# Kernel optimization log

Hardware: AMD Instinct MI355X
Metric: run time of the kernel (lower is better)

## Reference

```python
import jax, jax.numpy as jnp
import numpy as np

B, S, M = 32, 16384, 64
IN_DIM, OUT_DIM, HID = 64, 64, 512
N_READ, N_WRITE = 1, 1
LSTM_IN = IN_DIM + OUT_DIM + M * N_READ
EPS = 1e-8  # torch F.cosine_similarity eps


def setup_inputs():
    key = jax.random.key(0)
    ks = jax.random.split(key, 16)
    w = lambda k, sh: (0.02 * jax.random.normal(k, sh)).astype(jnp.float32)
    return {
        'x_input': jax.random.normal(ks[0], (B, 1, IN_DIM), dtype=jnp.float32),
        'prev_desired_output': jax.random.normal(ks[1], (B, 1, OUT_DIM), dtype=jnp.float32),
        'prev_read_vec': jax.random.normal(ks[2], (B, 1, M * N_READ), dtype=jnp.float32),
        'memory': jax.random.normal(ks[3], (B, S, M), dtype=jnp.float32),
        'W_ih': w(ks[4], (4 * HID, LSTM_IN)),
        'W_hh': w(ks[5], (4 * HID, HID)),
        'b_ih': jnp.zeros((4 * HID,), jnp.float32),
        'b_hh': jnp.zeros((4 * HID,), jnp.float32),
        'W_r': w(ks[6], (N_READ * (M + 6), HID)),
        'b_r': jnp.zeros((N_READ * (M + 6),), jnp.float32),
        'W_w': w(ks[7], (N_WRITE * (3 * M + 6), HID)),
        'b_w': jnp.zeros((N_WRITE * (3 * M + 6),), jnp.float32),
        'W_o': w(ks[8], (OUT_DIM, HID + M * N_READ)),
        'b_o': jnp.zeros((OUT_DIM,), jnp.float32),
    }


def _addressing(h, W, b, mem, nbr_heads, is_read):
    # ctrl2head linear -> [B, H, gate_dim], then slice k/beta/g/s/gamma(/erase/add)
    out = (h @ W.T + b).reshape(h.shape[0], nbr_heads, -1)
    k = out[..., :M]
    beta = jax.nn.softplus(out[..., M:M + 1])
    g = jax.nn.sigmoid(out[..., M + 1:M + 2])
    s = jax.nn.softmax(jax.nn.softplus(out[..., M + 2:M + 5]), axis=-1)  # 3-tap shift kernel
    gamma = 1.0 + jax.nn.softplus(out[..., M + 5:M + 6])
    # content addressing: cosine similarity of key vs each slot
    dot = jnp.einsum('bhm,bsm->bhs', k, mem)
    kn = jnp.maximum(jnp.linalg.norm(k, axis=-1), EPS)   # [B,H]
    mn = jnp.maximum(jnp.linalg.norm(mem, axis=-1), EPS)  # [B,S]
    cos = dot / (kn[:, :, None] * mn[:, None, :])
    wc = jax.nn.softmax(beta * cos, axis=-1)
    # location addressing; prev_w is zeros after reset so wg = g*wc + (1-g)*0
    wg = g * wc
    # circular 3-tap shift (conv1d over circularly padded weights)
    ws = s[..., 0:1] * jnp.roll(wg, 1, axis=-1) + s[..., 1:2] * wg + s[..., 2:3] * jnp.roll(wg, -1, axis=-1)
    wgam = ws ** gamma  # sharpening
    w_final = wgam / jnp.sum(wgam, axis=-1, keepdims=True)
    if is_read:
        return w_final
    return w_final, out[..., M + 6:2 * M + 6], out[..., 2 * M + 6:3 * M + 6]


def reference(x_input, prev_desired_output, prev_read_vec, memory,
              W_ih, W_hh, b_ih, b_hh, W_r, b_r, W_w, b_w, W_o, b_o):
    # single-layer LSTM step from zero (h0, c0) = (0, 0)
    xt = jnp.concatenate([x_input, prev_desired_output, prev_read_vec], axis=2)[:, 0]
    z = xt @ W_ih.T + b_ih + b_hh  # h0 @ W_hh.T == 0
    i, f, gg, o = jnp.split(z, 4, axis=-1)
    c = jax.nn.sigmoid(i) * jnp.tanh(gg)  # c0 == 0
    h = jax.nn.sigmoid(o) * jnp.tanh(c)   # [B, HID]
    # read heads (read pre-write memory)
    w_read = _addressing(h, W_r, b_r, memory, N_READ, True)
    r = jnp.einsum('bhs,bsm->bhm', w_read, memory)  # [B, N_READ, M]
    # write heads: source per-head loop overwrites nmemory[bidx] each head,
    # so only the LAST write head takes effect -> use head -1
    w_write, erase, add = _addressing(h, W_w, b_w, memory, N_WRITE, False)
    wl, el, al = w_write[:, -1], erase[:, -1], add[:, -1]
    new_mem = memory * (1.0 - wl[:, :, None] * el[:, None, :]) + wl[:, :, None] * al[:, None, :]
    # external output: softmax(Linear(cat(h, read)))
    ext_in = jnp.concatenate([h, r.reshape(r.shape[0], -1)], axis=-1)
    output = jax.nn.softmax(ext_in @ W_o.T + b_o, axis=-1)
    return output, new_mem
```

## Files before the change

kernel.cpp:

```cpp
#include <hip/hip_runtime.h>
#include <hip/hip_bf16.h>
#include <math.h>

#define BB 32
#define SS 16384
#define MM 64
#define HID 512
#define EPSV 1e-8f

#define OFF_H   0
#define OFF_P   16384
#define OFF_SER 32768
#define OFF_SEW 32800
#define OFF_SGR 32832
#define OFF_SGW 32864
#define OFF_R   32896
#define OFF_ER  40960
#define OFF_EW  (OFF_ER + BB*SS)
#define OFF_WGR (OFF_EW + BB*SS)
#define OFF_WGW (OFF_WGR + BB*SS)

__device__ __forceinline__ float sigmoidf_(float x) { return 1.f / (1.f + expf(-x)); }
__device__ __forceinline__ float softplusf_(float x) {
    return (x > 0.f) ? x + log1pf(expf(-x)) : log1pf(expf(x));
}

__global__ void k_lstm(const float* __restrict__ x, const float* __restrict__ pdo,
                       const float* __restrict__ prv,
                       const float* __restrict__ W_ih, const float* __restrict__ b_ih,
                       const float* __restrict__ b_hh, float* __restrict__ ws) {
    if (blockIdx.x == 0) {
        for (int i = threadIdx.x; i < 128 + BB * MM; i += 256) ws[OFF_SER + i] = 0.f;
    }
    int wid = blockIdx.x * 4 + (threadIdx.x >> 6);
    int lane = threadIdx.x & 63;
    int b = wid >> 9, t = wid & 511;
    float x0 = x[b * 64 + lane];
    float x1 = pdo[b * 64 + lane];
    float x2 = prv[b * 64 + lane];
    const float* wi = W_ih + (size_t)t * 192;
    const float* wg = W_ih + (size_t)(1024 + t) * 192;
    const float* wo = W_ih + (size_t)(1536 + t) * 192;
    float zi = x0 * wi[lane] + x1 * wi[64 + lane] + x2 * wi[128 + lane];
    float zg = x0 * wg[lane] + x1 * wg[64 + lane] + x2 * wg[128 + lane];
    float zo = x0 * wo[lane] + x1 * wo[64 + lane] + x2 * wo[128 + lane];
    #pragma unroll
    for (int off = 32; off >= 1; off >>= 1) {
        zi += __shfl_xor(zi, off);
        zg += __shfl_xor(zg, off);
        zo += __shfl_xor(zo, off);
    }
    if (lane == 0) {
        zi += b_ih[t] + b_hh[t];
        zg += b_ih[1024 + t] + b_hh[1024 + t];
        zo += b_ih[1536 + t] + b_hh[1536 + t];
        float c = sigmoidf_(zi) * tanhf(zg);
        ws[OFF_H + (size_t)b * 512 + t] = sigmoidf_(zo) * tanhf(c);
    }
}

__global__ void k_heads(const float* __restrict__ W_r, const float* __restrict__ b_r,
                        const float* __restrict__ W_w, const float* __restrict__ b_w,
                        float* __restrict__ ws) {
    int wid = blockIdx.x * 4 + (threadIdx.x >> 6);
    int lane = threadIdx.x & 63;
    int b = wid / 268, j = wid % 268;
    const float* h = ws + OFF_H + (size_t)b * 512;
    const float* wrow;
    float bias;
    if (j < 70) { wrow = W_r + (size_t)j * 512; bias = b_r[j]; }
    else        { wrow = W_w + (size_t)(j - 70) * 512; bias = b_w[j - 70]; }
    float acc = 0.f;
    #pragma unroll
    for (int c = 0; c < 8; c++) acc = fmaf(h[c * 64 + lane], wrow[c * 64 + lane], acc);
    #pragma unroll
    for (int off = 32; off >= 1; off >>= 1) acc += __shfl_xor(acc, off);
    if (lane != 0) return;
    acc += bias;
    float* P = ws + OFF_P + (size_t)b * 512;
    if (j < 70) {
        if (j < 64)       P[j] = acc;
        else if (j == 64) P[64] = softplusf_(acc);
        else if (j == 65) P[65] = sigmoidf_(acc);
        else if (j <= 68) P[96 + (j - 66)] = acc;
        else              P[69] = 1.f + softplusf_(acc);
    } else {
        int jj = j - 70;
        if (jj < 64)       P[128 + jj] = acc;
        else if (jj == 64) P[192] = softplusf_(acc);
        else if (jj == 65) P[193] = sigmoidf_(acc);
        else if (jj <= 68) P[224 + (jj - 66)] = acc;
        else if (jj == 69) P[197] = 1.f + softplusf_(acc);
        else if (jj < 134) P[256 + (jj - 70)] = acc;
        else               P[320 + (jj - 134)] = acc;
    }
}

__global__ void k_scorewgam(const float* __restrict__ mem, float* __restrict__ ws) {
    int b = blockIdx.x >> 6;
    int chunk = blockIdx.x & 63;
    int tid = threadIdx.x;
    const float* P = ws + OFF_P + (size_t)b * 512;

    __shared__ float sh_kr[64], sh_kw[64];
    __shared__ float sh_er[258], sh_ew[258];
    __shared__ float par[8];
    __shared__ float lr[4], lw[4];

    if (tid < 64) {
        float kr = P[tid], kw = P[128 + tid];
        sh_kr[tid] = kr; sh_kw[tid] = kw;
        float nr = kr * kr, nw = kw * kw;
        #pragma unroll
        for (int off = 32; off >= 1; off >>= 1) {
            nr += __shfl_xor(nr, off);
            nw += __shfl_xor(nw, off);
        }
        if (tid == 0) {
            par[0] = 1.f / fmaxf(sqrtf(nr), EPSV);
            par[1] = 1.f / fmaxf(sqrtf(nw), EPSV);
            float s0 = softplusf_(P[96]), s1 = softplusf_(P[97]), s2 = softplusf_(P[98]);
            float mx = fmaxf(s0, fmaxf(s1, s2));
            float e0 = expf(s0 - mx), e1 = expf(s1 - mx), e2 = expf(s2 - mx);
            float si = 1.f / (e0 + e1 + e2);
            par[2] = e0 * si; par[3] = e1 * si; par[4] = e2 * si;
            s0 = softplusf_(P[224]); s1 = softplusf_(P[225]); s2 = softplusf_(P[226]);
            mx = fmaxf(s0, fmaxf(s1, s2));
            e0 = expf(s0 - mx); e1 = expf(s1 - mx); e2 = expf(s2 - mx);
            si = 1.f / (e0 + e1 + e2);
            par[5] = e0 * si; par[6] = e1 * si; par[7] = e2 * si;
        }
    }
    float beta_r = P[64], beta_w = P[192];
    float gamma_r = P[69], gamma_w = P[197];
    __syncthreads();
    float ikr = par[0], ikw = par[1];

    int row0 = chunk * 256;
    {
        const float4* mrow = (const float4*)(mem + ((size_t)b * SS + row0 + tid) * 64);
        float dr = 0.f, dw = 0.f, n2 = 0.f;
        #pragma unroll
        for (int k = 0; k < 16; k++) {
            float4 m4 = mrow[k];
            float4 kr4 = *(const float4*)(sh_kr + k * 4);
            float4 kw4 = *(const float4*)(sh_kw + k * 4);
            dr = fmaf(m4.x, kr4.x, fmaf(m4.y, kr4.y, fmaf(m4.z, kr4.z, fmaf(m4.w, kr4.w, dr))));
            dw = fmaf(m4.x, kw4.x, fmaf(m4.y, kw4.y, fmaf(m4.z, kw4.z, fmaf(m4.w, kw4.w, dw))));
            n2 = fmaf(m4.x, m4.x, fmaf(m4.y, m4.y, fmaf(m4.z, m4.z, fmaf(m4.w, m4.w, n2))));
        }
        float imn = 1.f / fmaxf(sqrtf(n2), EPSV);
        sh_er[1 + tid] = exp2f(1.44269504f * beta_r * (dr * ikr * imn - 1.f));
        sh_ew[1 + tid] = exp2f(1.44269504f * beta_w * (dw * ikw * imn - 1.f));
    }
    if (tid < 32) {
        int grp = tid >> 4, c = tid & 15;
        int hrow = grp ? ((row0 + 256) & (SS - 1)) : ((row0 - 1) & (SS - 1));
        float4 m4 = *(const float4*)(mem + ((size_t)b * SS + hrow) * 64 + c * 4);
        float4 kr4 = *(const float4*)(sh_kr + c * 4);
        float4 kw4 = *(const float4*)(sh_kw + c * 4);
        float dr = m4.x * kr4.x + m4.y * kr4.y + m4.z * kr4.z + m4.w * kr4.w;
        float dw = m4.x * kw4.x + m4.y * kw4.y + m4.z * kw4.z + m4.w * kw4.w;
        float n2 = m4.x * m4.x + m4.y * m4.y + m4.z * m4.z + m4.w * m4.w;
        #pragma unroll
        for (int off = 8; off >= 1; off >>= 1) {
            dr += __shfl_xor(dr, off);
            dw += __shfl_xor(dw, off);
            n2 += __shfl_xor(n2, off);
        }
        if (c == 0) {
            float imn = 1.f / fmaxf(sqrtf(n2), EPSV);
            int slot = grp ? 257 : 0;
            sh_er[slot] = exp2f(1.44269504f * beta_r * (dr * ikr * imn - 1.f));
            sh_ew[slot] = exp2f(1.44269504f * beta_w * (dw * ikw * imn - 1.f));
        }
    }
    __syncthreads();

    float cvr = par[2] * sh_er[tid] + par[3] * sh_er[tid + 1] + par[4] * sh_er[tid + 2];
    float cvw = par[5] * sh_ew[tid] + par[6] * sh_ew[tid + 1] + par[7] * sh_ew[tid + 2];
    float wgr = exp2f(gamma_r * log2f(cvr));
    float wgw = exp2f(gamma_w * log2f(cvw));
    ws[OFF_WGR + (size_t)b * SS + row0 + tid] = wgr;
    ws[OFF_WGW + (size_t)b * SS + row0 + tid] = wgw;

    float rr = wgr, rw = wgw;
    #pragma unroll
    for (int off = 32; off >= 1; off >>= 1) {
        rr += __shfl_xor(rr, off);
        rw += __shfl_xor(rw, off);
    }
    int wv = tid >> 6, ln = tid & 63;
    if (ln == 0) { lr[wv] = rr; lw[wv] = rw; }
    __syncthreads();
    if (tid == 0) {
        atomicAdd(ws + OFF_SGR + b, lr[0] + lr[1] + lr[2] + lr[3]);
        atomicAdd(ws + OFF_SGW + b, lw[0] + lw[1] + lw[2] + lw[3]);
    }
}

__global__ void k_update(const float* __restrict__ mem, float* __restrict__ ws,
                         float* __restrict__ out) {
    int b = blockIdx.x >> 6, chunk = blockIdx.x & 63, tid = threadIdx.x;
    int rowslot = tid >> 4, col = tid & 15;
    const float* P = ws + OFF_P + (size_t)b * 512;
    float4 er4 = *(const float4*)(P + 256 + col * 4);
    float4 ad4 = *(const float4*)(P + 320 + col * 4);
    float isr = 1.f / ws[OFF_SGR + b];
    float isw = 1.f / ws[OFF_SGW + b];
    const float* wgr = ws + OFF_WGR + (size_t)b * SS;
    const float* wgw = ws + OFF_WGW + (size_t)b * SS;
    float* nm = out + 2048 + (size_t)b * SS * 64;
    float4 racc = {0.f, 0.f, 0.f, 0.f};
    int row0 = chunk * 256;
    for (int it = 0; it < 16; ++it) {
        int row = row0 + it * 16 + rowslot;
        float wr = wgr[row] * isr;
        float ww = wgw[row] * isw;
        float4 v = *(const float4*)(mem + ((size_t)b * SS + row) * 64 + col * 4);
        racc.x = fmaf(wr, v.x, racc.x);
        racc.y = fmaf(wr, v.y, racc.y);
        racc.z = fmaf(wr, v.z, racc.z);
        racc.w = fmaf(wr, v.w, racc.w);
        float4 o4;
        o4.x = v.x * (1.f - ww * er4.x) + ww * ad4.x;
        o4.y = v.y * (1.f - ww * er4.y) + ww * ad4.y;
        o4.z = v.z * (1.f - ww * er4.z) + ww * ad4.z;
        o4.w = v.w * (1.f - ww * er4.w) + ww * ad4.w;
        *(float4*)(nm + (size_t)row * 64 + col * 4) = o4;
    }
    __shared__ float4 red[256];
    red[tid] = racc;
    __syncthreads();
    if (tid < 16) {
        float4 a = red[tid];
        for (int rs = 1; rs < 16; ++rs) {
            float4 t2 = red[rs * 16 + tid];
            a.x += t2.x; a.y += t2.y; a.z += t2.z; a.w += t2.w;
        }
        atomicAdd(ws + OFF_R + b * 64 + tid * 4 + 0, a.x);
        atomicAdd(ws + OFF_R + b * 64 + tid * 4 + 1, a.y);
        atomicAdd(ws + OFF_R + b * 64 + tid * 4 + 2, a.z);
        atomicAdd(ws + OFF_R + b * 64 + tid * 4 + 3, a.w);
    }
}

__global__ void k_out(const float* __restrict__ ws, const float* __restrict__ W_o,
                      const float* __restrict__ b_o, float* __restrict__ out) {
    int b = blockIdx.x, o = threadIdx.x;
    const float* h = ws + OFF_H + (size_t)b * 512;
    const float* r = ws + OFF_R + (size_t)b * 64;
    const float* w = W_o + (size_t)o * 576;
    float acc = b_o[o];
    for (int t = 0; t < 512; t++) acc = fmaf(h[t], w[t], acc);
    for (int m = 0; m < 64; m++) acc = fmaf(r[m], w[512 + m], acc);
    float mx = acc;
    #pragma unroll
    for (int off = 32; off >= 1; off >>= 1) mx = fmaxf(mx, __shfl_xor(mx, off));
    float e = expf(acc - mx);
    float sm = e;
    #pragma unroll
    for (int off = 32; off >= 1; off >>= 1) sm += __shfl_xor(sm, off);
    out[b * 64 + o] = e / sm;
}

extern "C" void kernel_launch(void* const* d_in, const int* in_sizes, int n_in,
                              void* d_out, int out_size, void* d_ws, size_t ws_size,
                              hipStream_t stream) {
    const float* x    = (const float*)d_in[0];
    const float* pdo  = (const float*)d_in[1];
    const float* prv  = (const float*)d_in[2];
    const float* mem  = (const float*)d_in[3];
    const float* W_ih = (const float*)d_in[4];
    const float* b_ih = (const float*)d_in[6];
    const float* b_hh = (const float*)d_in[7];
    const float* W_r  = (const float*)d_in[8];
    const float* b_r  = (const float*)d_in[9];
    const float* W_w  = (const float*)d_in[10];
    const float* b_w  = (const float*)d_in[11];
    const float* W_o  = (const float*)d_in[12];
    const float* b_o  = (const float*)d_in[13];
    float* out = (float*)d_out;
    float* ws  = (float*)d_ws;

    k_lstm<<<BB * 512 / 4, 256, 0, stream>>>(x, pdo, prv, W_ih, b_ih, b_hh, ws);
    k_heads<<<(BB * 268) / 4, 256, 0, stream>>>(W_r, b_r, W_w, b_w, ws);
    k_scorewgam<<<BB * 64, 256, 0, stream>>>(mem, ws);
    k_update<<<BB * 64, 256, 0, stream>>>(mem, ws, out);
    k_out<<<BB, 64, 0, stream>>>(ws, W_o, b_o, out);
}
```

Baseline: 115.5 us.

## Coalesce scoring memory reads and replace atomics with per-chunk partial reductions

In the scoring kernel, each memory row is now read by 4 adjacent lanes, each loading 16 floats, with shuffle reductions. Before, one thread read a whole 256-byte row, so accesses across a wavefront were strided. The global atomicAdd accumulations for the weight sums and read vectors become per-chunk partial buffers that the consumer kernels sum. This also removes the zero-init step in the LSTM kernel. The cost is extra shuffles and a small serial reduction over 64 chunks in k_update and k_out.

```diff
diff --git a/kernel.cpp b/kernel.cpp
--- a/kernel.cpp
+++ b/kernel.cpp
@@ -8,17 +8,13 @@
 #define HID 512
 #define EPSV 1e-8f
 
-#define OFF_H   0
-#define OFF_P   16384
-#define OFF_SER 32768
-#define OFF_SEW 32800
-#define OFF_SGR 32832
-#define OFF_SGW 32864
-#define OFF_R   32896
-#define OFF_ER  40960
-#define OFF_EW  (OFF_ER + BB*SS)
-#define OFF_WGR (OFF_EW + BB*SS)
-#define OFF_WGW (OFF_WGR + BB*SS)
+#define OFF_H    0
+#define OFF_P    16384
+#define OFF_SGRP 32768
+#define OFF_SGWP (OFF_SGRP + BB*64)
+#define OFF_RP   (OFF_SGWP + BB*64)
+#define OFF_WGR  (OFF_RP + BB*64*64)
+#define OFF_WGW  (OFF_WGR + BB*SS)
 
 __device__ __forceinline__ float sigmoidf_(float x) { return 1.f / (1.f + expf(-x)); }
 __device__ __forceinline__ float softplusf_(float x) {
@@ -29,9 +25,6 @@
                        const float* __restrict__ prv,
                        const float* __restrict__ W_ih, const float* __restrict__ b_ih,
                        const float* __restrict__ b_hh, float* __restrict__ ws) {
-    if (blockIdx.x == 0) {
-        for (int i = threadIdx.x; i < 128 + BB * MM; i += 256) ws[OFF_SER + i] = 0.f;
-    }
     int wid = blockIdx.x * 4 + (threadIdx.x >> 6);
     int lane = threadIdx.x & 63;
     int b = wid >> 9, t = wid & 511;
@@ -135,24 +128,8 @@
     float gamma_r = P[69], gamma_w = P[197];
     __syncthreads();
     float ikr = par[0], ikw = par[1];
-
     int row0 = chunk * 256;
-    {
-        const float4* mrow = (const float4*)(mem + ((size_t)b * SS + row0 + tid) * 64);
-        float dr = 0.f, dw = 0.f, n2 = 0.f;
-        #pragma unroll
-        for (int k = 0; k < 16; k++) {
-            float4 m4 = mrow[k];
-            float4 kr4 = *(const float4*)(sh_kr + k * 4);
-            float4 kw4 = *(const float4*)(sh_kw + k * 4);
-            dr = fmaf(m4.x, kr4.x, fmaf(m4.y, kr4.y, fmaf(m4.z, kr4.z, fmaf(m4.w, kr4.w, dr))));
-            dw = fmaf(m4.x, kw4.x, fmaf(m4.y, kw4.y, fmaf(m4.z, kw4.z, fmaf(m4.w, kw4.w, dw))));
-            n2 = fmaf(m4.x, m4.x, fmaf(m4.y, m4.y, fmaf(m4.z, m4.z, fmaf(m4.w, m4.w, n2))));
-        }
-        float imn = 1.f / fmaxf(sqrtf(n2), EPSV);
-        sh_er[1 + tid] = exp2f(1.44269504f * beta_r * (dr * ikr * imn - 1.f));
-        sh_ew[1 + tid] = exp2f(1.44269504f * beta_w * (dw * ikw * imn - 1.f));
-    }
+
     if (tid < 32) {
         int grp = tid >> 4, c = tid & 15;
         int hrow = grp ? ((row0 + 256) & (SS - 1)) : ((row0 - 1) & (SS - 1));
@@ -175,6 +152,44 @@
             sh_ew[slot] = exp2f(1.44269504f * beta_w * (dw * ikw * imn - 1.f));
         }
     }
+
+    int w = tid >> 6, lane = tid & 63;
+    int rw = lane >> 2, q = lane & 3;
+    float4 kr0 = *(const float4*)(sh_kr + q * 16);
+    float4 kr1 = *(const float4*)(sh_kr + q * 16 + 4);
+    float4 kr2 = *(const float4*)(sh_kr + q * 16 + 8);
+    float4 kr3 = *(const float4*)(sh_kr + q * 16 + 12);
+    float4 kw0 = *(const float4*)(sh_kw + q * 16);
+    float4 kw1 = *(const float4*)(sh_kw + q * 16 + 4);
+    float4 kw2 = *(const float4*)(sh_kw + q * 16 + 8);
+    float4 kw3 = *(const float4*)(sh_kw + q * 16 + 12);
+    #pragma unroll 2
+    for (int it = 0; it < 4; ++it) {
+        int r = w * 64 + it * 16 + rw;
+        const float4* rp = (const float4*)(mem + ((size_t)b * SS + row0 + r) * 64) + q * 4;
+        float4 a0 = rp[0], a1 = rp[1], a2 = rp[2], a3 = rp[3];
+        float dr, dw, n2;
+        dr = a0.x*kr0.x + a0.y*kr0.y + a0.z*kr0.z + a0.w*kr0.w;
+        dr = fmaf(a1.x,kr1.x, fmaf(a1.y,kr1.y, fmaf(a1.z,kr1.z, fmaf(a1.w,kr1.w, dr))));
+        dr = fmaf(a2.x,kr2.x, fmaf(a2.y,kr2.y, fmaf(a2.z,kr2.z, fmaf(a2.w,kr2.w, dr))));
+        dr = fmaf(a3.x,kr3.x, fmaf(a3.y,kr3.y, fmaf(a3.z,kr3.z, fmaf(a3.w,kr3.w, dr))));
+        dw = a0.x*kw0.x + a0.y*kw0.y + a0.z*kw0.z + a0.w*kw0.w;
+        dw = fmaf(a1.x,kw1.x, fmaf(a1.y,kw1.y, fmaf(a1.z,kw1.z, fmaf(a1.w,kw1.w, dw))));
+        dw = fmaf(a2.x,kw2.x, fmaf(a2.y,kw2.y, fmaf(a2.z,kw2.z, fmaf(a2.w,kw2.w, dw))));
+        dw = fmaf(a3.x,kw3.x, fmaf(a3.y,kw3.y, fmaf(a3.z,kw3.z, fmaf(a3.w,kw3.w, dw))));
+        n2 = a0.x*a0.x + a0.y*a0.y + a0.z*a0.z + a0.w*a0.w;
+        n2 = fmaf(a1.x,a1.x, fmaf(a1.y,a1.y, fmaf(a1.z,a1.z, fmaf(a1.w,a1.w, n2))));
+        n2 = fmaf(a2.x,a2.x, fmaf(a2.y,a2.y, fmaf(a2.z,a2.z, fmaf(a2.w,a2.w, n2))));
+        n2 = fmaf(a3.x,a3.x, fmaf(a3.y,a3.y, fmaf(a3.z,a3.z, fmaf(a3.w,a3.w, n2))));
+        dr += __shfl_xor(dr, 1); dr += __shfl_xor(dr, 2);
+        dw += __shfl_xor(dw, 1); dw += __shfl_xor(dw, 2);
+        n2 += __shfl_xor(n2, 1); n2 += __shfl_xor(n2, 2);
+        if (q == 0) {
+            float imn = 1.f / fmaxf(sqrtf(n2), EPSV);
+            sh_er[1 + r] = exp2f(1.44269504f * beta_r * (dr * ikr * imn - 1.f));
+            sh_ew[1 + r] = exp2f(1.44269504f * beta_w * (dw * ikw * imn - 1.f));
+        }
+    }
     __syncthreads();
 
     float cvr = par[2] * sh_er[tid] + par[3] * sh_er[tid + 1] + par[4] * sh_er[tid + 2];
@@ -184,18 +199,17 @@
     ws[OFF_WGR + (size_t)b * SS + row0 + tid] = wgr;
     ws[OFF_WGW + (size_t)b * SS + row0 + tid] = wgw;
 
-    float rr = wgr, rw = wgw;
+    float rr = wgr, rw2 = wgw;
     #pragma unroll
     for (int off = 32; off >= 1; off >>= 1) {
         rr += __shfl_xor(rr, off);
-        rw += __shfl_xor(rw, off);
-    }
-    int wv = tid >> 6, ln = tid & 63;
-    if (ln == 0) { lr[wv] = rr; lw[wv] = rw; }
+        rw2 += __shfl_xor(rw2, off);
+    }
+    if (lane == 0) { lr[w] = rr; lw[w] = rw2; }
     __syncthreads();
     if (tid == 0) {
-        atomicAdd(ws + OFF_SGR + b, lr[0] + lr[1] + lr[2] + lr[3]);
-        atomicAdd(ws + OFF_SGW + b, lw[0] + lw[1] + lw[2] + lw[3]);
+        ws[OFF_SGRP + b * 64 + chunk] = lr[0] + lr[1] + lr[2] + lr[3];
+        ws[OFF_SGWP + b * 64 + chunk] = lw[0] + lw[1] + lw[2] + lw[3];
     }
 }
 
@@ -206,8 +220,22 @@
     const float* P = ws + OFF_P + (size_t)b * 512;
     float4 er4 = *(const float4*)(P + 256 + col * 4);
     float4 ad4 = *(const float4*)(P + 320 + col * 4);
-    float isr = 1.f / ws[OFF_SGR + b];
-    float isw = 1.f / ws[OFF_SGW + b];
+
+    __shared__ float sinv[2];
+    if (tid < 64) {
+        float v = ws[OFF_SGRP + b * 64 + tid];
+        #pragma unroll
+        for (int off = 32; off >= 1; off >>= 1) v += __shfl_xor(v, off);
+        if (tid == 0) sinv[0] = 1.f / v;
+    } else if (tid < 128) {
+        float v = ws[OFF_SGWP + b * 64 + (tid - 64)];
+        #pragma unroll
+        for (int off = 32; off >= 1; off >>= 1) v += __shfl_xor(v, off);
+        if (tid == 64) sinv[1] = 1.f / v;
+    }
+    __syncthreads();
+    float isr = sinv[0], isw = sinv[1];
+
     const float* wgr = ws + OFF_WGR + (size_t)b * SS;
     const float* wgw = ws + OFF_WGW + (size_t)b * SS;
     float* nm = out + 2048 + (size_t)b * SS * 64;
@@ -238,22 +266,27 @@
             float4 t2 = red[rs * 16 + tid];
             a.x += t2.x; a.y += t2.y; a.z += t2.z; a.w += t2.w;
         }
-        atomicAdd(ws + OFF_R + b * 64 + tid * 4 + 0, a.x);
-        atomicAdd(ws + OFF_R + b * 64 + tid * 4 + 1, a.y);
-        atomicAdd(ws + OFF_R + b * 64 + tid * 4 + 2, a.z);
-        atomicAdd(ws + OFF_R + b * 64 + tid * 4 + 3, a.w);
+        float* rp = ws + OFF_RP + ((size_t)b * 64 + chunk) * 64;
+        rp[tid * 4 + 0] = a.x;
+        rp[tid * 4 + 1] = a.y;
+        rp[tid * 4 + 2] = a.z;
+        rp[tid * 4 + 3] = a.w;
     }
 }
 
 __global__ void k_out(const float* __restrict__ ws, const float* __restrict__ W_o,
                       const float* __restrict__ b_o, float* __restrict__ out) {
     int b = blockIdx.x, o = threadIdx.x;
+    __shared__ float sh_r[64];
+    float accr = 0.f;
+    for (int c = 0; c < 64; ++c) accr += ws[OFF_RP + ((size_t)b * 64 + c) * 64 + o];
+    sh_r[o] = accr;
+    __syncthreads();
     const float* h = ws + OFF_H + (size_t)b * 512;
-    const float* r = ws + OFF_R + (size_t)b * 64;
     const float* w = W_o + (size_t)o * 576;
     float acc = b_o[o];
     for (int t = 0; t < 512; t++) acc = fmaf(h[t], w[t], acc);
-    for (int m = 0; m < 64; m++) acc = fmaf(r[m], w[512 + m], acc);
+    for (int m = 0; m < 64; m++) acc = fmaf(sh_r[m], w[512 + m], acc);
     float mx = acc;
     #pragma unroll
     for (int off = 32; off >= 1; off >>= 1) mx = fmaxf(mx, __shfl_xor(mx, off));
```

After: 97.01 us. -16.0%, faster.
